# Kernel optimization log

Measured on AMD Instinct MI355X. Metric: run time of the kernel, lower is better.

Reference implementation:

```python
import jax, jax.numpy as jnp
import numpy as np

N, D = 16384, 256

def setup_inputs() -> dict:
    key = jax.random.key(0)
    k1, k2 = jax.random.split(key)
    image_emb = jax.random.normal(k1, (N, D), dtype=jnp.float32)
    text_emb = jax.random.normal(k2, (N, D), dtype=jnp.float32)
    return {"image_emb": image_emb, "text_emb": text_emb}

def reference(image_emb, text_emb):
    n = image_emb.shape[0]
    # [n, n] similarity logits
    logits = image_emb @ text_emb.T
    labels = jnp.arange(n)
    # cross-entropy with diagonal labels: -log_softmax(logits)[i, i]
    logp_t = jax.nn.log_softmax(logits, axis=-1)        # image -> text (rows)
    logp_i = jax.nn.log_softmax(logits.T, axis=-1)      # text -> image (cols)
    loss_t = -logp_t[labels, labels]
    loss_i = -logp_i[labels, labels]
    loss = ((loss_i + loss_t) * 0.5).mean()
    return loss
```

## Files before the change

kernel.cpp:

```cpp
#include <hip/hip_runtime.h>
#include <hip/hip_bf16.h>

#define NN 16384
#define DD 256

typedef unsigned short u16;
typedef unsigned int u32;
typedef unsigned char u8;
typedef long i64;
typedef __attribute__((ext_vector_type(4))) float f32x4;
typedef __attribute__((ext_vector_type(4))) int i32x4;
typedef __attribute__((ext_vector_type(8))) int i32x8;

__global__ __launch_bounds__(256) void prep_kernel(
        const float* __restrict__ img, const float* __restrict__ txt,
        u8* __restrict__ A8, u8* __restrict__ B8,
        float* __restrict__ zbuf ,
        float* __restrict__ out) {
    __shared__ u32 sA[16 * 65 + 8];
    __shared__ u32 sB[16 * 65 + 8];
    const int t = threadIdx.x, bi = blockIdx.x;
    const float4* ib = (const float4*)img + ((size_t)bi << 10);
    const float4* tb = (const float4*)txt + ((size_t)bi << 10);
    const float S = 1.44269504088896f;
    #pragma unroll
    for (int k = 0; k < 4; ++k) {
        const int idx = (k << 8) + t;
        const int row = idx >> 6, col = idx & 63;
        float4 va = ib[idx];
        int pa = __builtin_amdgcn_cvt_pk_fp8_f32(va.x * S, va.y * S, 0, false);
        pa     = __builtin_amdgcn_cvt_pk_fp8_f32(va.z * S, va.w * S, pa, true);
        sA[row * 65 + col] = (u32)pa;
        float4 vb = tb[idx];
        int pb = __builtin_amdgcn_cvt_pk_fp8_f32(vb.x, vb.y, 0, false);
        pb     = __builtin_amdgcn_cvt_pk_fp8_f32(vb.z, vb.w, pb, true);
        sB[row * 65 + col] = (u32)pb;
    }
    __syncthreads();
    const int w = t >> 6, l = t & 63;
    const int k2 = w >> 1, jj = w & 1, qq = l >> 4, mm = l & 15;
    const int wb = mm * 65 + (k2 << 5) + (qq << 3) + (jj << 2);
    i32x4 oa = { (int)sA[wb], (int)sA[wb + 1], (int)sA[wb + 2], (int)sA[wb + 3] };
    i32x4 ob = { (int)sB[wb], (int)sB[wb + 1], (int)sB[wb + 2], (int)sB[wb + 3] };
    const size_t dst = ((size_t)(bi >> 3) << 15) + (k2 << 14) + ((size_t)(bi & 7) << 11)
                     + (jj << 10) + (qq << 8) + (mm << 4);
    *(i32x4*)(A8 + dst) = oa;
    *(i32x4*)(B8 + dst) = ob;
    const int gid = (bi << 8) + t;
    if (gid < 32768) zbuf[gid] = 0.0f;
    if (gid == 0) out[0] = 0.0f;
}

__global__ __launch_bounds__(256, 2) void gemm_lse_kernel(
        const u8* __restrict__ A8, const u8* __restrict__ B8,
        float* __restrict__ s_row, float* __restrict__ s_col,
        float* __restrict__ diag) {
    const int t = threadIdx.x;
    const int lane = t & 63;
    const int w = t >> 6;
    const int wr = w >> 1, wc = w & 1;
    const int q = lane >> 4, m = lane & 15;
    const int bi = blockIdx.x & 127;
    const int jg = blockIdx.x >> 7;
    const int row0 = bi << 7;

    const u8* Aw = A8 + ((size_t)bi << 15) + ((size_t)lane << 4);
    i32x8 areg[2][4];
    #pragma unroll
    for (int k2 = 0; k2 < 2; ++k2)
        #pragma unroll
        for (int rb = 0; rb < 4; ++rb) {
            const u8* p = Aw + (k2 << 14) + (((wr << 2) + rb) << 11);
            i32x4 lo = *(const i32x4*)(p);
            i32x4 hi = *(const i32x4*)(p + 1024);
            areg[k2][rb] = __builtin_shufflevector(lo, hi, 0, 1, 2, 3, 4, 5, 6, 7);
        }

    const f32x4 fzero = {0.f, 0.f, 0.f, 0.f};
    const f32x4 cinit = {-144.f, -144.f, -144.f, -144.f};
    f32x4 acc[4][4];
    f32x4 rp[4] = {fzero, fzero, fzero, fzero};

    const u8* Bw = B8 + (wc << 13) + ((size_t)lane << 4);

    i32x8 bfA[4], bfB[4];

    {
        const int ct0 = (jg << 4) | (bi & 15);
        const u8* p = Bw + ((size_t)ct0 << 15);
        #pragma unroll
        for (int cb = 0; cb < 4; ++cb) {
            i32x4 lo = *(const i32x4*)(p + (cb << 11));
            i32x4 hi = *(const i32x4*)(p + (cb << 11) + 1024);
            bfA[cb] = __builtin_shufflevector(lo, hi, 0, 1, 2, 3, 4, 5, 6, 7);
        }
    }

    #pragma unroll 1
    for (int jt = 0; jt < 16; ++jt) {
        const int ct = (jg << 4) | ((jt + bi) & 15);
        const int col0 = ct << 7;
        const u8* p = Bw + ((size_t)ct << 15);

        #pragma unroll
        for (int cb = 0; cb < 4; ++cb) {
            i32x4 lo = *(const i32x4*)(p + 16384 + (cb << 11));
            i32x4 hi = *(const i32x4*)(p + 16384 + (cb << 11) + 1024);
            bfB[cb] = __builtin_shufflevector(lo, hi, 0, 1, 2, 3, 4, 5, 6, 7);
        }

        __builtin_amdgcn_s_setprio(1);
        #pragma unroll
        for (int rb = 0; rb < 4; ++rb)
            #pragma unroll
            for (int cb = 0; cb < 4; ++cb)
                acc[rb][cb] = __builtin_amdgcn_mfma_scale_f32_16x16x128_f8f6f4(
                    areg[0][rb], bfA[cb], cinit, 0, 0, 0, 127, 0, 127);
        __builtin_amdgcn_s_setprio(0);

        if (jt < 15) {
            const int ctn = (jg << 4) | ((jt + 1 + bi) & 15);
            const u8* pn2 = Bw + ((size_t)ctn << 15);
            #pragma unroll
            for (int cb = 0; cb < 4; ++cb) {
                i32x4 lo = *(const i32x4*)(pn2 + (cb << 11));
                i32x4 hi = *(const i32x4*)(pn2 + (cb << 11) + 1024);
                bfA[cb] = __builtin_shufflevector(lo, hi, 0, 1, 2, 3, 4, 5, 6, 7);
            }
        }

        __builtin_amdgcn_s_setprio(1);
        #pragma unroll
        for (int rb = 0; rb < 4; ++rb)
            #pragma unroll
            for (int cb = 0; cb < 4; ++cb)
                acc[rb][cb] = __builtin_amdgcn_mfma_scale_f32_16x16x128_f8f6f4(
                    areg[1][rb], bfB[cb], acc[rb][cb], 0, 0, 0, 127, 0, 127);
        __builtin_amdgcn_s_setprio(0);

        if (bi == ct && wr == wc) {
            #pragma unroll
            for (int rb = 0; rb < 4; ++rb)
                #pragma unroll
                for (int r = 0; r < 4; ++r)
                    if (m == ((q << 2) | r))
                        diag[row0 + (wr << 6) + (rb << 4) + m] = acc[rb][rb][r];
        }
        #pragma unroll
        for (int rb = 0; rb < 4; ++rb)
            #pragma unroll
            for (int cb = 0; cb < 4; ++cb)
                #pragma unroll
                for (int r = 0; r < 4; ++r)
                    acc[rb][cb][r] = __builtin_amdgcn_exp2f(acc[rb][cb][r]);

        #pragma unroll
        for (int rb = 0; rb < 4; ++rb)
            rp[rb] += (acc[rb][0] + acc[rb][1]) + (acc[rb][2] + acc[rb][3]);

        float cpart = 0.0f;
        #pragma unroll
        for (int cb = 0; cb < 4; ++cb) {
            float v = 0.0f;
            #pragma unroll
            for (int rb = 0; rb < 4; ++rb)
                v += (acc[rb][cb][0] + acc[rb][cb][1]) + (acc[rb][cb][2] + acc[rb][cb][3]);
            v += __shfl_xor(v, 16, 64);
            v += __shfl_xor(v, 32, 64);
            if (q == cb) cpart = v;
        }
        atomicAdd(&s_col[col0 + (wc << 6) + (q << 4) + m], cpart);
    }

    float rout = 0.0f;
    #pragma unroll
    for (int rb = 0; rb < 4; ++rb)
        #pragma unroll
        for (int r = 0; r < 4; ++r) {
            float v = rp[rb][r];
            v += __shfl_xor(v, 1, 16);
            v += __shfl_xor(v, 2, 16);
            v += __shfl_xor(v, 4, 16);
            v += __shfl_xor(v, 8, 16);
            if (m == ((rb << 2) | r)) rout = v;
        }
    atomicAdd(&s_row[row0 + (wr << 6) + ((m >> 2) << 4) + (q << 2) + (m & 3)], rout);
}

__global__ void final_kernel(const float* __restrict__ s_row, const float* __restrict__ s_col,
                             const float* __restrict__ diag, float* __restrict__ out) {
    __shared__ double red[256];
    int t = threadIdx.x;
    int i = blockIdx.x * 256 + t;
    double p = 0.5 * (double)(log2f(s_row[i]) + log2f(s_col[i])) - (double)diag[i];
    red[t] = p;
    __syncthreads();
    for (int s = 128; s > 0; s >>= 1) {
        if (t < s) red[t] += red[t + s];
        __syncthreads();
    }
    if (t == 0) atomicAdd(out, (float)(red[0] * 0.6931471805599453 / (double)NN));
}

extern "C" void kernel_launch(void* const* d_in, const int* in_sizes, int n_in,
                              void* d_out, int out_size, void* d_ws, size_t ws_size,
                              hipStream_t stream) {
    const float* img = (const float*)d_in[0];
    const float* txt = (const float*)d_in[1];
    char* ws = (char*)d_ws;
    u8*    A8    = (u8*)ws;
    u8*    B8    = (u8*)(ws + 4194304);
    float* s_row = (float*)(ws + 8388608);
    float* s_col = (float*)(ws + 8388608 + 65536);
    float* diag  = (float*)(ws + 8388608 + 131072);
    float* out   = (float*)d_out;

    prep_kernel<<<1024, 256, 0, stream>>>(img, txt, A8, B8, s_row, out);
    gemm_lse_kernel<<<1024, 256, 0, stream>>>(A8, B8, s_row, s_col, diag);
    final_kernel<<<64, 256, 0, stream>>>(s_row, s_col, diag, out);
}
```

Before: 150.2 us.

## Ping-pong two accumulator sets to overlap MFMA with exp/reduction epilogue

Uses two accumulator arrays so the MFMA work for the next column tile is issued before the exp2 and reduction epilogue of the previous tile. The goal is to hide the epilogue's VALU and transcendental latency behind matrix-core work. B fragments are now loaded just in time inside each tile rather than prefetched one iteration ahead, and the setprio hints are dropped. The second accumulator set doubles accumulator register use, which risks spills or lower occupancy under launch_bounds(256,2).

```diff
diff --git a/kernel.cpp b/kernel.cpp
--- a/kernel.cpp
+++ b/kernel.cpp
@@ -77,67 +77,49 @@
         }
 
     const f32x4 fzero = {0.f, 0.f, 0.f, 0.f};
-    const f32x4 cinit = {-144.f, -144.f, -144.f, -144.f};
-    f32x4 acc[4][4];
+    f32x4 accA[4][4], accB[4][4];
     f32x4 rp[4] = {fzero, fzero, fzero, fzero};
 
     const u8* Bw = B8 + (wc << 13) + ((size_t)lane << 4);
 
-    i32x8 bfA[4], bfB[4];
-
-    {
-        const int ct0 = (jg << 4) | (bi & 15);
-        const u8* p = Bw + ((size_t)ct0 << 15);
-        #pragma unroll
-        for (int cb = 0; cb < 4; ++cb) {
-            i32x4 lo = *(const i32x4*)(p + (cb << 11));
-            i32x4 hi = *(const i32x4*)(p + (cb << 11) + 1024);
-            bfA[cb] = __builtin_shufflevector(lo, hi, 0, 1, 2, 3, 4, 5, 6, 7);
-        }
-    }
-
-    #pragma unroll 1
-    for (int jt = 0; jt < 16; ++jt) {
-        const int ct = (jg << 4) | ((jt + bi) & 15);
+    auto mfma_tile = [&](f32x4 (&acc)[4][4], int jt_) {
+        const int ct = (jg << 4) | ((jt_ + bi) & 15);
+        const u8* p = Bw + ((size_t)ct << 15);
+        const f32x4 cinit = {-144.f, -144.f, -144.f, -144.f};
+        #pragma unroll
+        for (int k2 = 0; k2 < 2; ++k2)
+            #pragma unroll
+            for (int cp = 0; cp < 2; ++cp) {
+                const u8* pp = p + (k2 << 14) + (cp << 12);
+                i32x4 lo0 = *(const i32x4*)(pp);
+                i32x4 hi0 = *(const i32x4*)(pp + 1024);
+                i32x8 bf0 = __builtin_shufflevector(lo0, hi0, 0, 1, 2, 3, 4, 5, 6, 7);
+                i32x4 lo1 = *(const i32x4*)(pp + 2048);
+                i32x4 hi1 = *(const i32x4*)(pp + 3072);
+                i32x8 bf1 = __builtin_shufflevector(lo1, hi1, 0, 1, 2, 3, 4, 5, 6, 7);
+                if (k2 == 0) {
+                    #pragma unroll
+                    for (int rb = 0; rb < 4; ++rb) {
+                        acc[rb][2 * cp]     = __builtin_amdgcn_mfma_scale_f32_16x16x128_f8f6f4(
+                            areg[0][rb], bf0, cinit, 0, 0, 0, 127, 0, 127);
+                        acc[rb][2 * cp + 1] = __builtin_amdgcn_mfma_scale_f32_16x16x128_f8f6f4(
+                            areg[0][rb], bf1, cinit, 0, 0, 0, 127, 0, 127);
+                    }
+                } else {
+                    #pragma unroll
+                    for (int rb = 0; rb < 4; ++rb) {
+                        acc[rb][2 * cp]     = __builtin_amdgcn_mfma_scale_f32_16x16x128_f8f6f4(
+                            areg[1][rb], bf0, acc[rb][2 * cp], 0, 0, 0, 127, 0, 127);
+                        acc[rb][2 * cp + 1] = __builtin_amdgcn_mfma_scale_f32_16x16x128_f8f6f4(
+                            areg[1][rb], bf1, acc[rb][2 * cp + 1], 0, 0, 0, 127, 0, 127);
+                    }
+                }
+            }
+    };
+
+    auto epilogue = [&](f32x4 (&acc)[4][4], int jt_) {
+        const int ct = (jg << 4) | ((jt_ + bi) & 15);
         const int col0 = ct << 7;
-        const u8* p = Bw + ((size_t)ct << 15);
-
-        #pragma unroll
-        for (int cb = 0; cb < 4; ++cb) {
-            i32x4 lo = *(const i32x4*)(p + 16384 + (cb << 11));
-            i32x4 hi = *(const i32x4*)(p + 16384 + (cb << 11) + 1024);
-            bfB[cb] = __builtin_shufflevector(lo, hi, 0, 1, 2, 3, 4, 5, 6, 7);
-        }
-
-        __builtin_amdgcn_s_setprio(1);
-        #pragma unroll
-        for (int rb = 0; rb < 4; ++rb)
-            #pragma unroll
-            for (int cb = 0; cb < 4; ++cb)
-                acc[rb][cb] = __builtin_amdgcn_mfma_scale_f32_16x16x128_f8f6f4(
-                    areg[0][rb], bfA[cb], cinit, 0, 0, 0, 127, 0, 127);
-        __builtin_amdgcn_s_setprio(0);
-
-        if (jt < 15) {
-            const int ctn = (jg << 4) | ((jt + 1 + bi) & 15);
-            const u8* pn2 = Bw + ((size_t)ctn << 15);
-            #pragma unroll
-            for (int cb = 0; cb < 4; ++cb) {
-                i32x4 lo = *(const i32x4*)(pn2 + (cb << 11));
-                i32x4 hi = *(const i32x4*)(pn2 + (cb << 11) + 1024);
-                bfA[cb] = __builtin_shufflevector(lo, hi, 0, 1, 2, 3, 4, 5, 6, 7);
-            }
-        }
-
-        __builtin_amdgcn_s_setprio(1);
-        #pragma unroll
-        for (int rb = 0; rb < 4; ++rb)
-            #pragma unroll
-            for (int cb = 0; cb < 4; ++cb)
-                acc[rb][cb] = __builtin_amdgcn_mfma_scale_f32_16x16x128_f8f6f4(
-                    areg[1][rb], bfB[cb], acc[rb][cb], 0, 0, 0, 127, 0, 127);
-        __builtin_amdgcn_s_setprio(0);
-
         if (bi == ct && wr == wc) {
             #pragma unroll
             for (int rb = 0; rb < 4; ++rb)
@@ -153,24 +135,32 @@
                 #pragma unroll
                 for (int r = 0; r < 4; ++r)
                     acc[rb][cb][r] = __builtin_amdgcn_exp2f(acc[rb][cb][r]);
-
         #pragma unroll
         for (int rb = 0; rb < 4; ++rb)
             rp[rb] += (acc[rb][0] + acc[rb][1]) + (acc[rb][2] + acc[rb][3]);
-
         float cpart = 0.0f;
         #pragma unroll
         for (int cb = 0; cb < 4; ++cb) {
-            float v = 0.0f;
-            #pragma unroll
-            for (int rb = 0; rb < 4; ++rb)
-                v += (acc[rb][cb][0] + acc[rb][cb][1]) + (acc[rb][cb][2] + acc[rb][cb][3]);
+            f32x4 s = (acc[0][cb] + acc[1][cb]) + (acc[2][cb] + acc[3][cb]);
+            float v = (s[0] + s[1]) + (s[2] + s[3]);
             v += __shfl_xor(v, 16, 64);
             v += __shfl_xor(v, 32, 64);
             if (q == cb) cpart = v;
         }
         atomicAdd(&s_col[col0 + (wc << 6) + (q << 4) + m], cpart);
+    };
+
+    mfma_tile(accA, 0);
+    #pragma unroll 1
+    for (int p7 = 0; p7 < 7; ++p7) {
+        mfma_tile(accB, 2 * p7 + 1);
+        epilogue (accA, 2 * p7);
+        mfma_tile(accA, 2 * p7 + 2);
+        epilogue (accB, 2 * p7 + 1);
     }
+    mfma_tile(accB, 15);
+    epilogue (accA, 14);
+    epilogue (accB, 15);
 
     float rout = 0.0f;
     #pragma unroll
```

Measured after the change: 394.0 us. 162% more time.
